# Performance work log

Measured on AMD Instinct MI355X. Metric: run time of the kernel, lower is better.

The kernel has to match this reference:

```python
import jax, jax.numpy as jnp
import numpy as np

HEADS = 4
DIM_HEAD = 64
DIM = 256
FMAP = 64
SCALE = DIM_HEAD ** -0.5


def setup_inputs() -> dict:
    key = jax.random.key(0)
    k1, k2, k3, k4 = jax.random.split(key, 4)
    inner = HEADS * DIM_HEAD
    fmap = jax.random.normal(k1, (4, DIM, FMAP, FMAP), dtype=jnp.float32)
    # 1x1 conv weight for qkv projection: (3*inner_dim, dim)
    w_qkv = jax.random.normal(k2, (3 * inner, DIM), dtype=jnp.float32) * (DIM ** -0.5)
    # AbsPosEmb parameters, initialized as randn * dim_head**-0.5 (as in BoTNet)
    pos_height = jax.random.normal(k3, (FMAP, DIM_HEAD), dtype=jnp.float32) * SCALE
    pos_width = jax.random.normal(k4, (FMAP, DIM_HEAD), dtype=jnp.float32) * SCALE
    return {"fmap": fmap, "w_qkv": w_qkv, "pos_height": pos_height, "pos_width": pos_width}


def reference(fmap, w_qkv, pos_height, pos_width):
    b, c, h, w = fmap.shape
    hw = h * w
    # 1x1 conv (no bias) == channel matmul
    qkv = jnp.einsum('bchw,oc->bohw', fmap, w_qkv)  # (b, 3*inner, h, w)
    q, k, v = jnp.split(qkv, 3, axis=1)
    # replicate torch .view(b, heads, h*w, -1): raw row-major reshape
    q = q.reshape(b, HEADS, hw, DIM_HEAD) * SCALE
    k = k.reshape(b, HEADS, hw, DIM_HEAD)
    v = v.reshape(b, HEADS, hw, DIM_HEAD)
    sim = jnp.einsum('bhid,bhjd->bhij', q, k)  # (b, heads, hw, hw)
    # absolute positional bias: emb[j] = height[y] + width[x], j = y*w + x
    emb = (pos_height[:, None, :] + pos_width[None, :, :]).reshape(hw, DIM_HEAD)
    sim = sim + jnp.einsum('bhid,jd->bhij', q, emb)
    attn = jax.nn.softmax(sim, axis=-1)
    out = jnp.einsum('bhij,bhjd->bhid', attn, v)  # (b, heads, hw, dim_head)
    # replicate torch .view(b, heads*dim_head, h, w): raw reshape
    return out.reshape(b, HEADS * DIM_HEAD, h, w)
```

## Files before the change

### kernel.cpp

```cpp
#include <hip/hip_runtime.h>


typedef float  f32x4  __attribute__((ext_vector_type(4)));
typedef __bf16 bf16x8 __attribute__((ext_vector_type(8)));
typedef __bf16 bf16x4 __attribute__((ext_vector_type(4)));

__device__ inline float fast_exp2(float x) {
#if __has_builtin(__builtin_amdgcn_exp2f)
  return __builtin_amdgcn_exp2f(x);
#else
  return exp2f(x);
#endif
}

__device__ inline void glds16(const __bf16* g, __bf16* l) {
  __builtin_amdgcn_global_load_lds(
      (const __attribute__((address_space(1))) void*)g,
      (__attribute__((address_space(3))) void*)l, 16, 0, 0);
}

__global__ __launch_bounds__(256) void w_cvt(
    const float* __restrict__ w, __bf16* __restrict__ wb)
{
  int idx = blockIdx.x * 256 + threadIdx.x;
  f32x4 v = ((const f32x4*)w)[idx];
  bf16x4 o; o[0]=(__bf16)v[0]; o[1]=(__bf16)v[1]; o[2]=(__bf16)v[2]; o[3]=(__bf16)v[3];
  ((bf16x4*)wb)[idx] = o;
}

__global__ __launch_bounds__(256) void qkv_proj(
    const float* __restrict__ fmap, const __bf16* __restrict__ wb,
    const float* __restrict__ ph,   const float* __restrict__ pw,
    __bf16* __restrict__ Qw, __bf16* __restrict__ Kw, __bf16* __restrict__ Vw)
{
  constexpr int LS = 264;
  __shared__ __bf16 Bs[32 * LS];
  const int tid  = threadIdx.x;
  const int wv   = tid >> 6;
  const int lane = tid & 63;
  const int quad = lane >> 4, l15 = lane & 15;
  const int n0 = blockIdx.x * 32;
  const int b  = blockIdx.y;

#pragma unroll
  for (int i = 0; i < 2; ++i) {
    int id = tid + i * 256;
    int ng = id & 7;
    int kg = id >> 3;
    const float* base = fmap + ((size_t)b * 256 + 4 * kg) * 4096 + n0 + 4 * ng;
    f32x4 v0 = *(const f32x4*)(base);
    f32x4 v1 = *(const f32x4*)(base + 4096);
    f32x4 v2 = *(const f32x4*)(base + 8192);
    f32x4 v3 = *(const f32x4*)(base + 12288);
#pragma unroll
    for (int j = 0; j < 4; ++j) {
      bf16x4 o; o[0]=(__bf16)v0[j]; o[1]=(__bf16)v1[j]; o[2]=(__bf16)v2[j]; o[3]=(__bf16)v3[j];
      *(bf16x4*)(&Bs[(4 * ng + j) * LS + 4 * kg]) = o;
    }
  }
  __syncthreads();

  for (int mt = 0; mt < 12; ++mt) {
    const int region = mt >> 2;
    const int obase  = (mt & 3) * 64;
    const __bf16* aptr = wb + (size_t)(mt * 64 + 16 * wv + l15) * 256 + 8 * quad;

    f32x4 acc[2] = {};
#pragma unroll
    for (int k0 = 0; k0 < 256; k0 += 32) {
      bf16x8 af = *(const bf16x8*)(aptr + k0);
      bf16x8 b0 = *(const bf16x8*)(&Bs[(l15)      * LS + k0 + 8 * quad]);
      bf16x8 b1 = *(const bf16x8*)(&Bs[(16 + l15) * LS + k0 + 8 * quad]);
      acc[0] = __builtin_amdgcn_mfma_f32_16x16x32_bf16(af, b0, acc[0], 0, 0, 0);
      acc[1] = __builtin_amdgcn_mfma_f32_16x16x32_bf16(af, b1, acc[1], 0, 0, 0);
    }

#pragma unroll
    for (int t = 0; t < 2; ++t) {
#pragma unroll
      for (int rr = 0; rr < 4; ++rr) {
        int oreg = obase + 16 * wv + 4 * quad + rr;
        int s    = n0 + 16 * t + l15;
        float val = acc[t][rr];
        size_t off = ((size_t)(b * 256 + oreg)) * 4096 + s;
        if (region == 0) {
          Qw[off] = (__bf16)(val * 0.18033688f);
        } else if (region == 1) {
          int g = oreg & 63;
          float bias = ph[g * 64 + (s & 63)] + pw[(s >> 6) * 64 + (s & 63)];
          Kw[off] = (__bf16)(val + bias);
        } else {
          Vw[off] = (__bf16)val;
        }
      }
    }
  }
}

__global__ __launch_bounds__(256) void v_transpose(
    const __bf16* __restrict__ Vw, __bf16* __restrict__ Vt)
{
  __shared__ __bf16 T[64 * 72];
  const int tid = threadIdx.x;
  const int j0  = blockIdx.x * 64;
  const int bh  = blockIdx.y;
  const __bf16* src = Vw + (size_t)bh * 262144;
#pragma unroll
  for (int i = 0; i < 2; ++i) {
    int id = tid + i * 256;
    int r = id >> 3, c = (id & 7) * 8;
    *(bf16x8*)(&T[r * 72 + c]) = *(const bf16x8*)(src + (size_t)(j0 + r) * 64 + c);
  }
  __syncthreads();
#pragma unroll
  for (int i = 0; i < 2; ++i) {
    int id = tid + i * 256;
    int d = id >> 3, jc = (id & 7) * 8;
    bf16x8 o;
#pragma unroll
    for (int z = 0; z < 8; ++z) o[z] = T[(jc + z) * 72 + d];
    *(bf16x8*)(Vt + ((size_t)bh * 64 + d) * 4096 + j0 + jc) = o;
  }
}

__global__ __launch_bounds__(256, 2) void flash_attn(
    const __bf16* __restrict__ Qg, const __bf16* __restrict__ Kg,
    const __bf16* __restrict__ Vtg, __bf16* __restrict__ OP0,
    float* __restrict__ lws, float* __restrict__ Og)
{
  __shared__ __bf16 Ks[2 * 64 * 64];
  __shared__ __bf16 Vs[2 * 64 * 64];
  const int tid  = threadIdx.x;
  const int wv   = tid >> 6;
  const int lane = tid & 63;
  const int quad = lane >> 4, l15 = lane & 15;
  const int bh = blockIdx.y;
  const int z  = blockIdx.z;
  const int iw = blockIdx.x * 256 + 64 * wv;
  const int jbase = z * 2048;
  const __bf16* Qb = Qg  + (size_t)bh * 262144;
  const __bf16* Kb = Kg  + (size_t)bh * 262144;
  const __bf16* Vb = Vtg + (size_t)bh * 262144;

  bf16x8 qf[4][2];
#pragma unroll
  for (int m = 0; m < 4; ++m)
#pragma unroll
    for (int c = 0; c < 2; ++c)
      qf[m][c] = *(const bf16x8*)(Qb + (size_t)(iw + 16 * m + l15) * 64 + 32 * c + 8 * quad);

  const int r0  = tid >> 3;
  const int kch = tid & 7;
  const int xc  = (kch ^ (r0 & 7)) * 8;
  const int pr0a = r0, pr1a = r0 + 32;
  const int pr0 = (pr0a & 0x23) | ((pr0a & 0x0C) << 1) | ((pr0a & 0x10) >> 2);
  const int pr1 = (pr1a & 0x23) | ((pr1a & 0x0C) << 1) | ((pr1a & 0x10) >> 2);
  const __bf16* kp0 = Kb + (size_t)(jbase + pr0) * 64 + xc;
  const __bf16* kp1 = Kb + (size_t)(jbase + pr1) * 64 + xc;
  const __bf16* vp0 = Vb + (size_t)r0 * 4096        + jbase + xc;
  const __bf16* vp1 = Vb + (size_t)(r0 + 32) * 4096 + jbase + xc;

  f32x4 acco[4][4] = {};
  f32x4 l4[4] = {};
  const int swz = (l15 & 7);

  auto dma_tile = [&](int buf) {
    __bf16* k0 = &Ks[buf * 4096 + tid * 8];
    __bf16* v0 = &Vs[buf * 4096 + tid * 8];
    glds16(kp0, k0);        kp0 += 4096;
    glds16(kp1, k0 + 2048); kp1 += 4096;
    glds16(vp0, v0);        vp0 += 64;
    glds16(vp1, v0 + 2048); vp1 += 64;
  };

  auto compute_tile = [&](int buf) {
    const __bf16* Kbuf = &Ks[buf * 4096];
    const __bf16* Vbuf = &Vs[buf * 4096];
    f32x4 sacc[4][4] = {};
#pragma unroll
    for (int c = 0; c < 2; ++c) {
#pragma unroll
      for (int t = 0; t < 4; ++t) {
        bf16x8 ak = *(const bf16x8*)(&Kbuf[(16 * t + l15) * 64 + (((4 * c + quad) ^ swz) * 8)]);
#pragma unroll
        for (int m = 0; m < 4; ++m)
          sacc[m][t] = __builtin_amdgcn_mfma_f32_16x16x32_bf16(ak, qf[m][c], sacc[m][t], 0, 0, 0);
      }
    }
    bf16x8 pf[4][2];
#pragma unroll
    for (int m = 0; m < 4; ++m) {
#pragma unroll
      for (int t = 0; t < 4; ++t) {
#pragma unroll
        for (int r = 0; r < 4; ++r) {
          float pv = fast_exp2(sacc[m][t][r]);
          sacc[m][t][r] = pv;
          l4[m][r] += pv;
        }
      }
#pragma unroll
      for (int c2 = 0; c2 < 2; ++c2) {
        bf16x8 a;
#pragma unroll
        for (int r = 0; r < 4; ++r) {
          a[r]     = (__bf16)sacc[m][2 * c2][r];
          a[4 + r] = (__bf16)sacc[m][2 * c2 + 1][r];
        }
        pf[m][c2] = a;
      }
    }
#pragma unroll
    for (int c2 = 0; c2 < 2; ++c2) {
#pragma unroll
      for (int t = 0; t < 4; ++t) {
        bf16x8 bv = *(const bf16x8*)(&Vbuf[(16 * t + l15) * 64 + (((4 * c2 + quad) ^ swz) * 8)]);
#pragma unroll
        for (int m = 0; m < 4; ++m)
          acco[m][t] = __builtin_amdgcn_mfma_f32_16x16x32_bf16(pf[m][c2], bv, acco[m][t], 0, 0, 0);
      }
    }
  };

  dma_tile(0);
  for (int it = 0; it < 32; it += 2) {
    __syncthreads();
    dma_tile(1);
    compute_tile(0);
    __syncthreads();
    if (it < 30) dma_tile(0);
    compute_tile(1);
  }

#pragma unroll
  for (int m = 0; m < 4; ++m) {
    float l = (l4[m][0] + l4[m][1]) + (l4[m][2] + l4[m][3]);
    l += __shfl_xor(l, 16, 64);
    l += __shfl_xor(l, 32, 64);
    if (quad == 0)
      lws[z * 65536 + bh * 4096 + iw + 16 * m + l15] = l;
  }
  if (z == 0) {
    __bf16* Ob = OP0 + (size_t)bh * 262144;
#pragma unroll
    for (int m = 0; m < 4; ++m)
#pragma unroll
      for (int t = 0; t < 4; ++t)
#pragma unroll
        for (int r = 0; r < 4; ++r)
          Ob[(size_t)(iw + 16 * m + 4 * quad + r) * 64 + 16 * t + l15] =
              (__bf16)acco[m][t][r];
  } else {
    float* Ob = Og + (size_t)bh * 262144;
#pragma unroll
    for (int m = 0; m < 4; ++m)
#pragma unroll
      for (int t = 0; t < 4; ++t)
#pragma unroll
        for (int r = 0; r < 4; ++r)
          Ob[(size_t)(iw + 16 * m + 4 * quad + r) * 64 + 16 * t + l15] =
              acco[m][t][r];
  }
}

__global__ __launch_bounds__(256) void combine(
    const __bf16* __restrict__ OP0, const float* __restrict__ lws,
    float* __restrict__ Og)
{
  int idx = blockIdx.x * 256 + threadIdx.x;
  int row = idx >> 4;
  float inv = 1.0f / (lws[row] + lws[65536 + row]);
  f32x4 o = ((const f32x4*)Og)[idx];
  bf16x4 p = ((const bf16x4*)OP0)[idx];
  f32x4 r;
#pragma unroll
  for (int k = 0; k < 4; ++k) r[k] = (o[k] + (float)p[k]) * inv;
  ((f32x4*)Og)[idx] = r;
}

extern "C" void kernel_launch(void* const* d_in, const int* in_sizes, int n_in,
                              void* d_out, int out_size, void* d_ws, size_t ws_size,
                              hipStream_t stream) {
  const float* fmap = (const float*)d_in[0];
  const float* w    = (const float*)d_in[1];
  const float* ph   = (const float*)d_in[2];
  const float* pw   = (const float*)d_in[3];
  float* out = (float*)d_out;

  __bf16* Qw = (__bf16*)d_ws;
  __bf16* Kw = Qw + 4194304;
  __bf16* Vw = Kw + 4194304;
  __bf16* Vt = Vw + 4194304;
  float*  lws = (float*)(Vt + 4194304);
  __bf16* Wb16 = (__bf16*)(lws + 131072);

  w_cvt      <<<dim3(192),       256, 0, stream>>>(w, Wb16);
  qkv_proj   <<<dim3(128, 4),    256, 0, stream>>>(fmap, Wb16, ph, pw, Qw, Kw, Vw);
  v_transpose<<<dim3(64, 16),    256, 0, stream>>>(Vw, Vt);
  flash_attn <<<dim3(16, 16, 2), 256, 0, stream>>>(Qw, Kw, Vt, Vw , lws, out);
  combine    <<<dim3(4096),      256, 0, stream>>>(Vw , lws, out);
}
```

Before: 183.4 us.

## Double K/V tile depth, compute row sums via MFMA, add setprio hints

Each pipeline stage now loads 128 keys instead of 64, halving the number of barrier-separated iterations. The softmax denominator is accumulated with an extra MFMA against a ones vector instead of per-element VALU adds. s_setprio raises wave priority around the MFMA phases so matrix work can interleave with other waves' exp phases. This doubles LDS use per block and sums bf16-rounded probabilities rather than fp32 ones.

```diff
diff --git a/kernel.cpp b/kernel.cpp
--- a/kernel.cpp
+++ b/kernel.cpp
@@ -128,8 +128,8 @@
     const __bf16* __restrict__ Vtg, __bf16* __restrict__ OP0,
     float* __restrict__ lws, float* __restrict__ Og)
 {
-  __shared__ __bf16 Ks[2 * 64 * 64];
-  __shared__ __bf16 Vs[2 * 64 * 64];
+  __shared__ __bf16 Ks[2 * 128 * 64];
+  __shared__ __bf16 Vs[2 * 128 * 64];
   const int tid  = threadIdx.x;
   const int wv   = tid >> 6;
   const int lane = tid & 63;
@@ -161,22 +161,31 @@
   const __bf16* vp1 = Vb + (size_t)(r0 + 32) * 4096 + jbase + xc;
 
   f32x4 acco[4][4] = {};
-  f32x4 l4[4] = {};
+  f32x4 lacc[4] = {};
   const int swz = (l15 & 7);
 
+  bf16x8 onesb;
+#pragma unroll
+  for (int r = 0; r < 8; ++r) onesb[r] = (__bf16)1.0f;
+
   auto dma_tile = [&](int buf) {
-    __bf16* k0 = &Ks[buf * 4096 + tid * 8];
-    __bf16* v0 = &Vs[buf * 4096 + tid * 8];
-    glds16(kp0, k0);        kp0 += 4096;
-    glds16(kp1, k0 + 2048); kp1 += 4096;
-    glds16(vp0, v0);        vp0 += 64;
-    glds16(vp1, v0 + 2048); vp1 += 64;
+    __bf16* k0 = &Ks[buf * 8192 + tid * 8];
+    __bf16* v0 = &Vs[buf * 8192 + tid * 8];
+    glds16(kp0, k0);         kp0 += 4096;
+    glds16(kp1, k0 + 2048);  kp1 += 4096;
+    glds16(vp0, v0);         vp0 += 64;
+    glds16(vp1, v0 + 2048);  vp1 += 64;
+    glds16(kp0, k0 + 4096);  kp0 += 4096;
+    glds16(kp1, k0 + 6144);  kp1 += 4096;
+    glds16(vp0, v0 + 4096);  vp0 += 64;
+    glds16(vp1, v0 + 6144);  vp1 += 64;
   };
 
-  auto compute_tile = [&](int buf) {
-    const __bf16* Kbuf = &Ks[buf * 4096];
-    const __bf16* Vbuf = &Vs[buf * 4096];
+  auto compute_tile = [&](int buf, int sub) {
+    const __bf16* Kbuf = &Ks[buf * 8192 + sub * 4096];
+    const __bf16* Vbuf = &Vs[buf * 8192 + sub * 4096];
     f32x4 sacc[4][4] = {};
+    __builtin_amdgcn_s_setprio(1);
 #pragma unroll
     for (int c = 0; c < 2; ++c) {
 #pragma unroll
@@ -187,18 +196,15 @@
           sacc[m][t] = __builtin_amdgcn_mfma_f32_16x16x32_bf16(ak, qf[m][c], sacc[m][t], 0, 0, 0);
       }
     }
+    __builtin_amdgcn_s_setprio(0);
     bf16x8 pf[4][2];
 #pragma unroll
     for (int m = 0; m < 4; ++m) {
 #pragma unroll
-      for (int t = 0; t < 4; ++t) {
-#pragma unroll
-        for (int r = 0; r < 4; ++r) {
-          float pv = fast_exp2(sacc[m][t][r]);
-          sacc[m][t][r] = pv;
-          l4[m][r] += pv;
-        }
-      }
+      for (int t = 0; t < 4; ++t)
+#pragma unroll
+        for (int r = 0; r < 4; ++r)
+          sacc[m][t][r] = fast_exp2(sacc[m][t][r]);
 #pragma unroll
       for (int c2 = 0; c2 < 2; ++c2) {
         bf16x8 a;
@@ -210,6 +216,7 @@
         pf[m][c2] = a;
       }
     }
+    __builtin_amdgcn_s_setprio(1);
 #pragma unroll
     for (int c2 = 0; c2 < 2; ++c2) {
 #pragma unroll
@@ -219,26 +226,32 @@
         for (int m = 0; m < 4; ++m)
           acco[m][t] = __builtin_amdgcn_mfma_f32_16x16x32_bf16(pf[m][c2], bv, acco[m][t], 0, 0, 0);
       }
-    }
+#pragma unroll
+      for (int m = 0; m < 4; ++m)
+        lacc[m] = __builtin_amdgcn_mfma_f32_16x16x32_bf16(pf[m][c2], onesb, lacc[m], 0, 0, 0);
+    }
+    __builtin_amdgcn_s_setprio(0);
   };
 
   dma_tile(0);
-  for (int it = 0; it < 32; it += 2) {
+  for (int it = 0; it < 16; it += 2) {
     __syncthreads();
     dma_tile(1);
-    compute_tile(0);
+    compute_tile(0, 0);
+    compute_tile(0, 1);
     __syncthreads();
-    if (it < 30) dma_tile(0);
-    compute_tile(1);
+    if (it < 14) dma_tile(0);
+    compute_tile(1, 0);
+    compute_tile(1, 1);
   }
 
 #pragma unroll
   for (int m = 0; m < 4; ++m) {
-    float l = (l4[m][0] + l4[m][1]) + (l4[m][2] + l4[m][3]);
-    l += __shfl_xor(l, 16, 64);
-    l += __shfl_xor(l, 32, 64);
-    if (quad == 0)
-      lws[z * 65536 + bh * 4096 + iw + 16 * m + l15] = l;
+    if (l15 == 0) {
+#pragma unroll
+      for (int r = 0; r < 4; ++r)
+        lws[z * 65536 + bh * 4096 + iw + 16 * m + 4 * quad + r] = lacc[m][r];
+    }
   }
   if (z == 0) {
     __bf16* Ob = OP0 + (size_t)bh * 262144;
```

Result: faster. 177.1 us (-3.4%).
